# Optimization experiments

Hardware: AMD Instinct MI355X
Metric: run time of the kernel (lower is better)

The kernel has to match this reference:

```python
import jax, jax.numpy as jnp
import numpy as np

HS = 4096   # hidden_size
IS = 2048   # input_size (also number of output classes)
T, B = 4, 1 # seq_len * batch MUST equal 4 (output.view(4,-1) constraint)


def setup_inputs() -> dict:
    key = jax.random.key(0)
    ks = jax.random.split(key, 5)
    inp = jax.random.normal(ks[0], (T, B, IS), dtype=jnp.float32)
    target = jax.random.randint(ks[1], (T * B, 1), 0, IS)
    # xavier-style init for 2D params, zeros for bias-like (per init_weights)
    weight = jax.random.normal(ks[2], (4 * HS, IS + HS), dtype=jnp.float32) * np.float32(1.0 / np.sqrt(IS + HS))
    bias = jnp.zeros((4 * HS, 1), dtype=jnp.float32)
    W = jax.random.normal(ks[3], (IS, HS), dtype=jnp.float32) * np.float32(1.0 / np.sqrt(HS))
    b = jnp.zeros((IS, 1), dtype=jnp.float32)
    return {"input": inp, "target": target, "weight": weight, "bias": bias, "W": W, "b": b}


def reference(input, target, weight, bias, W, b):
    hs = weight.shape[0] // 4
    seq_len, batch, _ = input.shape
    h0 = jnp.zeros((hs, batch), dtype=input.dtype)
    c0 = jnp.zeros((hs, batch), dtype=input.dtype)

    def step(carry, x_t):
        h, c = carry
        z = jnp.concatenate([h, x_t.T], axis=0)          # [HS+IS, B]
        g = weight @ z + bias                            # [4*HS, B]
        f = jax.nn.sigmoid(g[:hs])
        i = jax.nn.sigmoid(g[hs:2 * hs])
        c_bar = jnp.tanh(g[2 * hs:3 * hs])
        o = jax.nn.sigmoid(g[3 * hs:])
        c = c * f + c_bar * i
        h = jnp.tanh(c) * o
        return (h, c), h

    _, outs = jax.lax.scan(step, (h0, c0), input)        # outs: [T, HS, B]
    # transpose(2,1) then view(4,-1): valid only when T*B == 4
    out = outs.transpose(0, 2, 1).reshape(4, -1)          # [4, HS]
    logits = (W @ out.T + b).T                            # [4, IS]
    logp = jax.nn.log_softmax(logits, axis=1)             # stable softmax+log
    rows = jnp.arange(logits.shape[0])
    # loss = sum over rows of -log softmax at target class (scatter one-hot * pred)
    loss = -jnp.sum(logp[rows, target[:, 0]])
    return loss
```

## Files before the change

### kernel.cpp

```cpp
#include <hip/hip_runtime.h>
#include <math.h>

#define HS 4096
#define IS 2048
#define NT 4
#define NR 16384
#define ZD 6144

__device__ __forceinline__ float wave_reduce(float v) {
#pragma unroll
    for (int off = 32; off > 0; off >>= 1) v += __shfl_xor(v, off, 64);
    return v;
}

__device__ __forceinline__ float sigf(float x) { return 1.0f / (1.0f + expf(-x)); }

__global__ __launch_bounds__(256) void gx_kernel(
    const float* __restrict__ x,
    const float* __restrict__ weight,
    const float* __restrict__ bias,
    float* __restrict__ Gx)
{
    __shared__ float xs[NT * IS];
    const int tid = threadIdx.x;
    for (int i = tid; i < NT * IS; i += 256) xs[i] = x[i];
    __syncthreads();

    const int wave = tid >> 6, lane = tid & 63;
    const int r = blockIdx.x * 4 + wave;
    const float4* wrow = reinterpret_cast<const float4*>(weight + (size_t)r * ZD + HS);
    const float4* xs4 = reinterpret_cast<const float4*>(xs);

    float a0 = 0.f, a1 = 0.f, a2 = 0.f, a3 = 0.f;
#pragma unroll
    for (int it = 0; it < (IS / 4) / 64; ++it) {
        const int e = it * 64 + lane;
        const float4 w = wrow[e];
        const float4 p = xs4[e];
        const float4 q = xs4[(IS / 4) + e];
        const float4 s = xs4[2 * (IS / 4) + e];
        const float4 u = xs4[3 * (IS / 4) + e];
        a0 += w.x * p.x + w.y * p.y + w.z * p.z + w.w * p.w;
        a1 += w.x * q.x + w.y * q.y + w.z * q.z + w.w * q.w;
        a2 += w.x * s.x + w.y * s.y + w.z * s.z + w.w * s.w;
        a3 += w.x * u.x + w.y * u.y + w.z * u.z + w.w * u.w;
    }
    a0 = wave_reduce(a0); a1 = wave_reduce(a1);
    a2 = wave_reduce(a2); a3 = wave_reduce(a3);
    if (lane == 0) {
        const float bb = bias[r];
        Gx[0 * NR + r] = a0 + bb;
        Gx[1 * NR + r] = a1 + bb;
        Gx[2 * NR + r] = a2 + bb;
        Gx[3 * NR + r] = a3 + bb;
    }
}

__global__ __launch_bounds__(256) void step0_kernel(
    const float* __restrict__ Gx,
    float* __restrict__ H0,
    float* __restrict__ cvec)
{
    const int j = blockIdx.x * 256 + threadIdx.x;
    const float gi = Gx[HS + j];
    const float gc = Gx[2 * HS + j];
    const float go = Gx[3 * HS + j];
    const float cn = tanhf(gc) * sigf(gi);
    cvec[j] = cn;
    H0[j] = tanhf(cn) * sigf(go);
}

__global__ __launch_bounds__(256) void steph_kernel(
    const float* __restrict__ weight,
    const float* __restrict__ Gx,
    const float* __restrict__ Hprev,
    float* __restrict__ Hout,
    float* __restrict__ cvec,
    const int t)
{
    __shared__ float hs_[HS];
    const int tid = threadIdx.x;
    for (int i = tid; i < HS; i += 256) hs_[i] = Hprev[i];
    __syncthreads();

    const int wave = tid >> 6, lane = tid & 63;
    const int j = blockIdx.x * 4 + wave;
    const float4* h4 = reinterpret_cast<const float4*>(hs_);

    float acc[4];
#pragma unroll
    for (int k = 0; k < 4; ++k) {
        const float4* wrow = reinterpret_cast<const float4*>(weight + (size_t)(k * HS + j) * ZD);
        float a = 0.f;
#pragma unroll
        for (int it = 0; it < (HS / 4) / 64; ++it) {
            const int e = it * 64 + lane;
            const float4 w = wrow[e];
            const float4 h = h4[e];
            a += w.x * h.x + w.y * h.y + w.z * h.z + w.w * h.w;
        }
        acc[k] = a;
    }
#pragma unroll
    for (int k = 0; k < 4; ++k) acc[k] = wave_reduce(acc[k]);

    if (lane == 0) {
        const size_t gb = (size_t)t * NR;
        const float gf = acc[0] + Gx[gb + j];
        const float gi = acc[1] + Gx[gb + HS + j];
        const float gc = acc[2] + Gx[gb + 2 * HS + j];
        const float go = acc[3] + Gx[gb + 3 * HS + j];
        const float cn = cvec[j] * sigf(gf) + tanhf(gc) * sigf(gi);
        cvec[j] = cn;
        Hout[j] = tanhf(cn) * sigf(go);
    }
}

__global__ __launch_bounds__(256) void logits_kernel(
    const float* __restrict__ W,
    const float* __restrict__ bvec,
    const float* __restrict__ H,
    float* __restrict__ logits)
{
    const int wave = threadIdx.x >> 6, lane = threadIdx.x & 63;
    const int r = blockIdx.x * 4 + wave;
    const float4* wrow = reinterpret_cast<const float4*>(W + (size_t)r * HS);
    const float4* H4 = reinterpret_cast<const float4*>(H);

    float acc[4] = {0.f, 0.f, 0.f, 0.f};
#pragma unroll
    for (int it = 0; it < (HS / 4) / 64; ++it) {
        const int e = it * 64 + lane;
        const float4 w = wrow[e];
#pragma unroll
        for (int t = 0; t < 4; ++t) {
            const float4 h = H4[t * (HS / 4) + e];
            acc[t] += w.x * h.x + w.y * h.y + w.z * h.z + w.w * h.w;
        }
    }
#pragma unroll
    for (int t = 0; t < 4; ++t) acc[t] = wave_reduce(acc[t]);
    if (lane == 0) {
        const float bv = bvec[r];
#pragma unroll
        for (int t = 0; t < 4; ++t) logits[t * IS + r] = acc[t] + bv;
    }
}

__global__ __launch_bounds__(256) void loss_kernel(
    const float* __restrict__ logits,
    const int* __restrict__ target,
    float* __restrict__ out)
{
    __shared__ float red[256];
    const int tid = threadIdx.x;
    float total = 0.f;
    for (int t = 0; t < NT; ++t) {
        const float* row = logits + t * IS;
        float m = -1e30f;
        for (int r = tid; r < IS; r += 256) m = fmaxf(m, row[r]);
        red[tid] = m;
        __syncthreads();
        for (int s = 128; s > 0; s >>= 1) {
            if (tid < s) red[tid] = fmaxf(red[tid], red[tid + s]);
            __syncthreads();
        }
        m = red[0];
        __syncthreads();
        float sum = 0.f;
        for (int r = tid; r < IS; r += 256) sum += expf(row[r] - m);
        red[tid] = sum;
        __syncthreads();
        for (int s = 128; s > 0; s >>= 1) {
            if (tid < s) red[tid] += red[tid + s];
            __syncthreads();
        }
        if (tid == 0) {
            const float lse = m + logf(red[0]);
            total += lse - row[target[t]];
        }
        __syncthreads();
    }
    if (tid == 0) out[0] = total;
}

extern "C" void kernel_launch(void* const* d_in, const int* in_sizes, int n_in,
                              void* d_out, int out_size, void* d_ws, size_t ws_size,
                              hipStream_t stream) {
    const float* x      = (const float*)d_in[0];
    const int*   target = (const int*)  d_in[1];
    const float* weight = (const float*)d_in[2];
    const float* bias   = (const float*)d_in[3];
    const float* W      = (const float*)d_in[4];
    const float* bvec   = (const float*)d_in[5];
    float* out = (float*)d_out;

    float* ws = (float*)d_ws;
    float* Gx     = ws;
    float* H      = ws + 65536;
    float* cvec   = ws + 65536 + 16384;
    float* logits = ws + 65536 + 16384 + 4096;

    hipLaunchKernelGGL(gx_kernel, dim3(NR / 4), dim3(256), 0, stream, x, weight, bias, Gx);
    hipLaunchKernelGGL(step0_kernel, dim3(HS / 256), dim3(256), 0, stream, Gx, H, cvec);
    for (int t = 1; t < NT; ++t) {
        hipLaunchKernelGGL(steph_kernel, dim3(HS / 4), dim3(256), 0, stream,
                           weight, Gx, H + (size_t)(t - 1) * HS, H + (size_t)t * HS, cvec, t);
    }
    hipLaunchKernelGGL(logits_kernel, dim3(IS / 4), dim3(256), 0, stream, W, bvec, H, logits);
    hipLaunchKernelGGL(loss_kernel, dim3(1), dim3(256), 0, stream, logits, target, out);
}
```

Before: 192.4 us.

## Fuse LSTM into one persistent cooperative kernel with on-chip fp16 weights

Replaces the six launches with a single cooperative kernel of 256 blocks. Each block loads its slice of the recurrent weights once, converts it to fp16 and keeps it in registers and LDS for all timesteps. Grid syncs separate the steps, the logits GEMV and the loss. The goal is to stop re-reading the large weight matrix from HBM at every step and to remove launch overhead, at the cost of fp16 rounding error in the recurrent weights and heavy register pressure.

```diff
diff --git a/kernel.cpp b/kernel.cpp
--- a/kernel.cpp
+++ b/kernel.cpp
@@ -1,187 +1,227 @@
 #include <hip/hip_runtime.h>
+#include <hip/hip_fp16.h>
+#include <hip/hip_cooperative_groups.h>
 #include <math.h>
+
+namespace cg = cooperative_groups;
 
 #define HS 4096
 #define IS 2048
 #define NT 4
-#define NR 16384
 #define ZD 6144
+
+typedef float fvec4 __attribute__((ext_vector_type(4)));
 
 __device__ __forceinline__ float wave_reduce(float v) {
 #pragma unroll
     for (int off = 32; off > 0; off >>= 1) v += __shfl_xor(v, off, 64);
     return v;
 }
-
 __device__ __forceinline__ float sigf(float x) { return 1.0f / (1.0f + expf(-x)); }
 
-__global__ __launch_bounds__(256) void gx_kernel(
+static __device__ __forceinline__ float4 ldnt(const float4* p) {
+    fvec4 v = __builtin_nontemporal_load(reinterpret_cast<const fvec4*>(p));
+    return make_float4(v.x, v.y, v.z, v.w);
+}
+
+union U2H { uint2 u; __half2 h[2]; };
+
+__global__ __launch_bounds__(512, 2) void lstm_all(
     const float* __restrict__ x,
+    const int* __restrict__ target,
     const float* __restrict__ weight,
     const float* __restrict__ bias,
-    float* __restrict__ Gx)
-{
-    __shared__ float xs[NT * IS];
-    const int tid = threadIdx.x;
-    for (int i = tid; i < NT * IS; i += 256) xs[i] = x[i];
-    __syncthreads();
-
-    const int wave = tid >> 6, lane = tid & 63;
-    const int r = blockIdx.x * 4 + wave;
-    const float4* wrow = reinterpret_cast<const float4*>(weight + (size_t)r * ZD + HS);
-    const float4* xs4 = reinterpret_cast<const float4*>(xs);
-
-    float a0 = 0.f, a1 = 0.f, a2 = 0.f, a3 = 0.f;
-#pragma unroll
-    for (int it = 0; it < (IS / 4) / 64; ++it) {
-        const int e = it * 64 + lane;
-        const float4 w = wrow[e];
-        const float4 p = xs4[e];
-        const float4 q = xs4[(IS / 4) + e];
-        const float4 s = xs4[2 * (IS / 4) + e];
-        const float4 u = xs4[3 * (IS / 4) + e];
-        a0 += w.x * p.x + w.y * p.y + w.z * p.z + w.w * p.w;
-        a1 += w.x * q.x + w.y * q.y + w.z * q.z + w.w * q.w;
-        a2 += w.x * s.x + w.y * s.y + w.z * s.z + w.w * s.w;
-        a3 += w.x * u.x + w.y * u.y + w.z * u.z + w.w * u.w;
-    }
-    a0 = wave_reduce(a0); a1 = wave_reduce(a1);
-    a2 = wave_reduce(a2); a3 = wave_reduce(a3);
-    if (lane == 0) {
-        const float bb = bias[r];
-        Gx[0 * NR + r] = a0 + bb;
-        Gx[1 * NR + r] = a1 + bb;
-        Gx[2 * NR + r] = a2 + bb;
-        Gx[3 * NR + r] = a3 + bb;
-    }
-}
-
-__global__ __launch_bounds__(256) void step0_kernel(
-    const float* __restrict__ Gx,
-    float* __restrict__ H0,
-    float* __restrict__ cvec)
-{
-    const int j = blockIdx.x * 256 + threadIdx.x;
-    const float gi = Gx[HS + j];
-    const float gc = Gx[2 * HS + j];
-    const float go = Gx[3 * HS + j];
-    const float cn = tanhf(gc) * sigf(gi);
-    cvec[j] = cn;
-    H0[j] = tanhf(cn) * sigf(go);
-}
-
-__global__ __launch_bounds__(256) void steph_kernel(
-    const float* __restrict__ weight,
-    const float* __restrict__ Gx,
-    const float* __restrict__ Hprev,
-    float* __restrict__ Hout,
-    float* __restrict__ cvec,
-    const int t)
-{
-    __shared__ float hs_[HS];
-    const int tid = threadIdx.x;
-    for (int i = tid; i < HS; i += 256) hs_[i] = Hprev[i];
-    __syncthreads();
-
-    const int wave = tid >> 6, lane = tid & 63;
-    const int j = blockIdx.x * 4 + wave;
-    const float4* h4 = reinterpret_cast<const float4*>(hs_);
-
-    float acc[4];
-#pragma unroll
-    for (int k = 0; k < 4; ++k) {
-        const float4* wrow = reinterpret_cast<const float4*>(weight + (size_t)(k * HS + j) * ZD);
-        float a = 0.f;
-#pragma unroll
-        for (int it = 0; it < (HS / 4) / 64; ++it) {
-            const int e = it * 64 + lane;
-            const float4 w = wrow[e];
-            const float4 h = h4[e];
-            a += w.x * h.x + w.y * h.y + w.z * h.z + w.w * h.w;
-        }
-        acc[k] = a;
-    }
-#pragma unroll
-    for (int k = 0; k < 4; ++k) acc[k] = wave_reduce(acc[k]);
-
-    if (lane == 0) {
-        const size_t gb = (size_t)t * NR;
-        const float gf = acc[0] + Gx[gb + j];
-        const float gi = acc[1] + Gx[gb + HS + j];
-        const float gc = acc[2] + Gx[gb + 2 * HS + j];
-        const float go = acc[3] + Gx[gb + 3 * HS + j];
-        const float cn = cvec[j] * sigf(gf) + tanhf(gc) * sigf(gi);
-        cvec[j] = cn;
-        Hout[j] = tanhf(cn) * sigf(go);
-    }
-}
-
-__global__ __launch_bounds__(256) void logits_kernel(
     const float* __restrict__ W,
     const float* __restrict__ bvec,
-    const float* __restrict__ H,
+    float* __restrict__ out,
+    float* __restrict__ H,
     float* __restrict__ logits)
 {
-    const int wave = threadIdx.x >> 6, lane = threadIdx.x & 63;
-    const int r = blockIdx.x * 4 + wave;
-    const float4* wrow = reinterpret_cast<const float4*>(W + (size_t)r * HS);
-    const float4* H4 = reinterpret_cast<const float4*>(H);
-
-    float acc[4] = {0.f, 0.f, 0.f, 0.f};
-#pragma unroll
-    for (int it = 0; it < (HS / 4) / 64; ++it) {
-        const int e = it * 64 + lane;
-        const float4 w = wrow[e];
-#pragma unroll
-        for (int t = 0; t < 4; ++t) {
-            const float4 h = H4[t * (HS / 4) + e];
-            acc[t] += w.x * h.x + w.y * h.y + w.z * h.z + w.w * h.w;
-        }
-    }
-#pragma unroll
-    for (int t = 0; t < 4; ++t) acc[t] = wave_reduce(acc[t]);
-    if (lane == 0) {
-        const float bv = bvec[r];
-#pragma unroll
-        for (int t = 0; t < 4; ++t) logits[t * IS + r] = acc[t] + bv;
-    }
-}
-
-__global__ __launch_bounds__(256) void loss_kernel(
-    const float* __restrict__ logits,
-    const int* __restrict__ target,
-    float* __restrict__ out)
-{
-    __shared__ float red[256];
+    __shared__ uint2 wlds[16 * 1024];
+    __shared__ __align__(16) float hbuf[HS];
+    __shared__ float gxbuf[8][2][4][4];
+    __shared__ float cvs[16];
+    __shared__ float red[512];
+
     const int tid = threadIdx.x;
-    float total = 0.f;
-    for (int t = 0; t < NT; ++t) {
-        const float* row = logits + t * IS;
-        float m = -1e30f;
-        for (int r = tid; r < IS; r += 256) m = fmaxf(m, row[r]);
-        red[tid] = m;
+    const int w = tid >> 6, l = tid & 63;
+    const int b = blockIdx.x;
+    const int u0 = b * 16 + 2 * w;
+    cg::grid_group grid = cg::this_grid();
+
+    int rid[8];
+    rid[0] = 0 * HS + u0;     rid[1] = 1 * HS + u0;     rid[2] = 2 * HS + u0;
+    rid[3] = 0 * HS + u0 + 1; rid[4] = 1 * HS + u0 + 1; rid[5] = 2 * HS + u0 + 1;
+    rid[6] = 3 * HS + u0;     rid[7] = 3 * HS + u0 + 1;
+    const int gate_of[8] = {0, 1, 2, 0, 1, 2, 3, 3};
+    const int unit_of[8] = {0, 0, 0, 1, 1, 1, 0, 1};
+
+    __half2 wst[6][16][2];
+
+#pragma unroll
+    for (int r = 0; r < 8; ++r) {
+        const float* wrow = weight + (size_t)rid[r] * ZD;
+        const float4* wr4 = reinterpret_cast<const float4*>(wrow);
+        if (r < 6) {
+#pragma unroll
+            for (int j = 0; j < 16; ++j) {
+                float4 v = ldnt(&wr4[64 * j + l]);
+                wst[r][j][0] = __floats2half2_rn(v.x, v.y);
+                wst[r][j][1] = __floats2half2_rn(v.z, v.w);
+            }
+        } else {
+            uint2* dst = wlds + (size_t)(2 * w + (r - 6)) * 1024;
+#pragma unroll
+            for (int j = 0; j < 16; ++j) {
+                float4 v = ldnt(&wr4[64 * j + l]);
+                U2H pk;
+                pk.h[0] = __floats2half2_rn(v.x, v.y);
+                pk.h[1] = __floats2half2_rn(v.z, v.w);
+                dst[64 * j + l] = pk.u;
+            }
+        }
+        const float4* xr4 = reinterpret_cast<const float4*>(wrow + HS);
+        const float4* xv4 = reinterpret_cast<const float4*>(x);
+        float a0 = 0.f, a1 = 0.f, a2 = 0.f, a3 = 0.f;
+#pragma unroll
+        for (int i = 0; i < 8; ++i) {
+            float4 wv = ldnt(&xr4[64 * i + l]);
+            float4 x0 = xv4[0 * 512 + 64 * i + l];
+            float4 x1 = xv4[1 * 512 + 64 * i + l];
+            float4 x2 = xv4[2 * 512 + 64 * i + l];
+            float4 x3 = xv4[3 * 512 + 64 * i + l];
+            a0 += wv.x * x0.x + wv.y * x0.y + wv.z * x0.z + wv.w * x0.w;
+            a1 += wv.x * x1.x + wv.y * x1.y + wv.z * x1.z + wv.w * x1.w;
+            a2 += wv.x * x2.x + wv.y * x2.y + wv.z * x2.z + wv.w * x2.w;
+            a3 += wv.x * x3.x + wv.y * x3.y + wv.z * x3.z + wv.w * x3.w;
+        }
+        a0 = wave_reduce(a0); a1 = wave_reduce(a1);
+        a2 = wave_reduce(a2); a3 = wave_reduce(a3);
+        if (l == 0) {
+            const float bb = bias[rid[r]];
+            gxbuf[w][unit_of[r]][gate_of[r]][0] = a0 + bb;
+            gxbuf[w][unit_of[r]][gate_of[r]][1] = a1 + bb;
+            gxbuf[w][unit_of[r]][gate_of[r]][2] = a2 + bb;
+            gxbuf[w][unit_of[r]][gate_of[r]][3] = a3 + bb;
+        }
+    }
+    __syncthreads();
+
+    if (l == 0) {
+#pragma unroll
+        for (int ui = 0; ui < 2; ++ui) {
+            const int u = u0 + ui;
+            const float gi = gxbuf[w][ui][1][0];
+            const float gc = gxbuf[w][ui][2][0];
+            const float go = gxbuf[w][ui][3][0];
+            const float cn = tanhf(gc) * sigf(gi);
+            cvs[2 * w + ui] = cn;
+            H[u] = tanhf(cn) * sigf(go);
+        }
+    }
+    grid.sync();
+
+    for (int t = 1; t < NT; ++t) {
+        const float4* hp4 = reinterpret_cast<const float4*>(H + (size_t)(t - 1) * HS);
+        float4* hb4 = reinterpret_cast<float4*>(hbuf);
+        for (int i = tid; i < HS / 4; i += 512) hb4[i] = hp4[i];
         __syncthreads();
-        for (int s = 128; s > 0; s >>= 1) {
-            if (tid < s) red[tid] = fmaxf(red[tid], red[tid + s]);
-            __syncthreads();
-        }
-        m = red[0];
-        __syncthreads();
-        float sum = 0.f;
-        for (int r = tid; r < IS; r += 256) sum += expf(row[r] - m);
-        red[tid] = sum;
-        __syncthreads();
-        for (int s = 128; s > 0; s >>= 1) {
-            if (tid < s) red[tid] += red[tid + s];
-            __syncthreads();
-        }
-        if (tid == 0) {
-            const float lse = m + logf(red[0]);
-            total += lse - row[target[t]];
-        }
-        __syncthreads();
-    }
-    if (tid == 0) out[0] = total;
+
+        float acc[8];
+#pragma unroll
+        for (int r = 0; r < 8; ++r) acc[r] = 0.f;
+#pragma unroll
+        for (int j = 0; j < 16; ++j) {
+            const float4 h4 = hb4[64 * j + l];
+#pragma unroll
+            for (int r = 0; r < 6; ++r) {
+                const __half2 p = wst[r][j][0], q = wst[r][j][1];
+                acc[r] += __low2float(p) * h4.x + __high2float(p) * h4.y
+                        + __low2float(q) * h4.z + __high2float(q) * h4.w;
+            }
+#pragma unroll
+            for (int r = 6; r < 8; ++r) {
+                U2H pk;
+                pk.u = wlds[(size_t)(2 * w + (r - 6)) * 1024 + 64 * j + l];
+                acc[r] += __low2float(pk.h[0]) * h4.x + __high2float(pk.h[0]) * h4.y
+                        + __low2float(pk.h[1]) * h4.z + __high2float(pk.h[1]) * h4.w;
+            }
+        }
+#pragma unroll
+        for (int r = 0; r < 8; ++r) acc[r] = wave_reduce(acc[r]);
+
+        if (l == 0) {
+#pragma unroll
+            for (int ui = 0; ui < 2; ++ui) {
+                const int u = u0 + ui;
+                const float gf = (ui ? acc[3] : acc[0]) + gxbuf[w][ui][0][t];
+                const float gi = (ui ? acc[4] : acc[1]) + gxbuf[w][ui][1][t];
+                const float gc = (ui ? acc[5] : acc[2]) + gxbuf[w][ui][2][t];
+                const float go = (ui ? acc[7] : acc[6]) + gxbuf[w][ui][3][t];
+                const float cn = cvs[2 * w + ui] * sigf(gf) + tanhf(gc) * sigf(gi);
+                cvs[2 * w + ui] = cn;
+                H[(size_t)t * HS + u] = tanhf(cn) * sigf(go);
+            }
+        }
+        grid.sync();
+    }
+
+    {
+        const int row = b * 8 + w;
+        const float4* wr4 = reinterpret_cast<const float4*>(W + (size_t)row * HS);
+        const float4* H4 = reinterpret_cast<const float4*>(H);
+        float a0 = 0.f, a1 = 0.f, a2 = 0.f, a3 = 0.f;
+#pragma unroll
+        for (int i = 0; i < 16; ++i) {
+            const float4 wv = ldnt(&wr4[64 * i + l]);
+            const float4 h0 = H4[0 * 1024 + 64 * i + l];
+            const float4 h1 = H4[1 * 1024 + 64 * i + l];
+            const float4 h2 = H4[2 * 1024 + 64 * i + l];
+            const float4 h3 = H4[3 * 1024 + 64 * i + l];
+            a0 += wv.x * h0.x + wv.y * h0.y + wv.z * h0.z + wv.w * h0.w;
+            a1 += wv.x * h1.x + wv.y * h1.y + wv.z * h1.z + wv.w * h1.w;
+            a2 += wv.x * h2.x + wv.y * h2.y + wv.z * h2.z + wv.w * h2.w;
+            a3 += wv.x * h3.x + wv.y * h3.y + wv.z * h3.z + wv.w * h3.w;
+        }
+        a0 = wave_reduce(a0); a1 = wave_reduce(a1);
+        a2 = wave_reduce(a2); a3 = wave_reduce(a3);
+        if (l == 0) {
+            const float bv = bvec[row];
+            logits[0 * IS + row] = a0 + bv;
+            logits[1 * IS + row] = a1 + bv;
+            logits[2 * IS + row] = a2 + bv;
+            logits[3 * IS + row] = a3 + bv;
+        }
+    }
+    grid.sync();
+
+    if (b == 0) {
+        float total = 0.f;
+        for (int t = 0; t < NT; ++t) {
+            const float* row = logits + (size_t)t * IS;
+            float m = -1e30f;
+            for (int r = tid; r < IS; r += 512) m = fmaxf(m, row[r]);
+            red[tid] = m;
+            __syncthreads();
+            for (int s = 256; s > 0; s >>= 1) {
+                if (tid < s) red[tid] = fmaxf(red[tid], red[tid + s]);
+                __syncthreads();
+            }
+            m = red[0];
+            __syncthreads();
+            float sum = 0.f;
+            for (int r = tid; r < IS; r += 512) sum += expf(row[r] - m);
+            red[tid] = sum;
+            __syncthreads();
+            for (int s = 256; s > 0; s >>= 1) {
+                if (tid < s) red[tid] += red[tid + s];
+                __syncthreads();
+            }
+            if (tid == 0) total += (m + logf(red[0])) - row[target[t]];
+            __syncthreads();
+        }
+        if (tid == 0) out[0] = total;
+    }
 }
 
 extern "C" void kernel_launch(void* const* d_in, const int* in_sizes, int n_in,
@@ -195,18 +235,10 @@
     const float* bvec   = (const float*)d_in[5];
     float* out = (float*)d_out;
 
-    float* ws = (float*)d_ws;
-    float* Gx     = ws;
-    float* H      = ws + 65536;
-    float* cvec   = ws + 65536 + 16384;
-    float* logits = ws + 65536 + 16384 + 4096;
-
-    hipLaunchKernelGGL(gx_kernel, dim3(NR / 4), dim3(256), 0, stream, x, weight, bias, Gx);
-    hipLaunchKernelGGL(step0_kernel, dim3(HS / 256), dim3(256), 0, stream, Gx, H, cvec);
-    for (int t = 1; t < NT; ++t) {
-        hipLaunchKernelGGL(steph_kernel, dim3(HS / 4), dim3(256), 0, stream,
-                           weight, Gx, H + (size_t)(t - 1) * HS, H + (size_t)t * HS, cvec, t);
-    }
-    hipLaunchKernelGGL(logits_kernel, dim3(IS / 4), dim3(256), 0, stream, W, bvec, H, logits);
-    hipLaunchKernelGGL(loss_kernel, dim3(1), dim3(256), 0, stream, logits, target, out);
-}
+    float* H      = (float*)d_ws;
+    float* logits = (float*)d_ws + 4 * HS;
+
+    void* args[] = {(void*)&x, (void*)&target, (void*)&weight, (void*)&bias,
+                    (void*)&W, (void*)&bvec, (void*)&out, (void*)&H, (void*)&logits};
+    (void)hipLaunchCooperativeKernel((void*)lstm_all, dim3(256), dim3(512), args, 0, stream);
+}
```

Result: slower. 524.1 us (+172.4%).
